# Performance work log

Measured on AMD Instinct MI355X. Metric: run time of the kernel, lower is better.

The kernel has to match this reference:

```python
import jax, jax.numpy as jnp
import numpy as np

B, T, C = 4, 4096, 1024
NEG_INF = -1e38


def setup_inputs() -> dict:
    key = jax.random.key(0)
    ks = jax.random.split(key, 5)
    scale = 0.02  # realistic init scale for CxC projections
    x = jax.random.normal(ks[0], (B, T, C), dtype=jnp.float32)
    key_w = jax.random.normal(ks[1], (C, C), dtype=jnp.float32) * scale
    value_w = jax.random.normal(ks[2], (C, C), dtype=jnp.float32) * scale
    receptance_w = jax.random.normal(ks[3], (C, C), dtype=jnp.float32) * scale
    output_w = jax.random.normal(ks[4], (C, C), dtype=jnp.float32) * scale
    # deterministic param init matching the module's __init__
    time_decay = -5.0 + 8.0 * (jnp.arange(C, dtype=jnp.float32) / (C - 1)) ** 0.7
    time_first = jnp.full((C,), -3.0, dtype=jnp.float32)
    # initial WKV state as in forward() when state is None
    aa0 = jnp.zeros((B, C), dtype=jnp.float32)
    bb0 = jnp.zeros((B, C), dtype=jnp.float32)
    pp0 = jnp.full((B, C), NEG_INF, dtype=jnp.float32)
    return dict(x=x, key_w=key_w, value_w=value_w, receptance_w=receptance_w,
                output_w=output_w, time_decay=time_decay, time_first=time_first,
                aa0=aa0, bb0=bb0, pp0=pp0)


def reference(x, key_w, value_w, receptance_w, output_w,
              time_decay, time_first, aa0, bb0, pp0):
    # projections (torch Linear: y = x @ W.T)
    k = jnp.einsum('btc,dc->btd', x, key_w)        # [B,T,C]
    v = jnp.einsum('btc,dc->btd', x, value_w)      # [B,T,C]
    r = jax.nn.sigmoid(jnp.einsum('btc,dc->btd', x, receptance_w))
    w = jnp.exp(time_decay)  # [C]
    u = time_first           # [C]

    def step(carry, kv):
        aa, bb, pp = carry           # each [B,C]
        kt, vt = kv                  # each [B,C]
        # output at this step (numerically stabilized exp weighting)
        ww = u + kt
        p = jnp.maximum(pp, ww)
        e1 = jnp.exp(pp - p)
        e2 = jnp.exp(ww - p)
        wkv = (e1 * aa + e2 * vt) / (e1 * bb + e2)
        # state update
        ww2 = pp - w
        p2 = jnp.maximum(ww2, kt)
        e1b = jnp.exp(ww2 - p2)
        e2b = jnp.exp(kt - p2)
        return (e1b * aa + e2b * vt, e1b * bb + e2b, p2), wkv

    k_t = jnp.swapaxes(k, 0, 1)  # [T,B,C]
    v_t = jnp.swapaxes(v, 0, 1)
    (aa, bb, pp), wkv = jax.lax.scan(step, (aa0, bb0, pp0), (k_t, v_t))
    wkv = jnp.swapaxes(wkv, 0, 1)  # [B,T,C]

    out = jnp.einsum('btc,dc->btd', r * wkv, output_w)
    return out, aa, bb, pp
```

## Files before the change

kernel.cpp:

```cpp
#include <hip/hip_runtime.h>
#include <stdint.h>

#define BDIM 4
#define TDIM 4096
#define CDIM 1024
#define MDIM (BDIM * TDIM)
#define SSEG 64
#define LSEG 64
#define NCH  (BDIM * CDIM)

#define GK   1024
#define GK2  2048
#define NTK  16
#define NT4  64

typedef __attribute__((ext_vector_type(8))) short bf16x8;
typedef __attribute__((ext_vector_type(4))) float f32x4;

__device__ __forceinline__ unsigned short f2bf(float f) {
    unsigned u = __builtin_bit_cast(unsigned, f);
    u = u + 0x7fffu + ((u >> 16) & 1u);
    return (unsigned short)(u >> 16);
}
__device__ __forceinline__ float bf2f(unsigned short h) {
    unsigned u = ((unsigned)h) << 16;
    return __builtin_bit_cast(float, u);
}

typedef __attribute__((address_space(1))) const unsigned int g_u32;
typedef __attribute__((address_space(3))) unsigned int l_u32;
__device__ __forceinline__ void gload_lds16(const void* g, void* l) {
    __builtin_amdgcn_global_load_lds((g_u32*)g, (l_u32*)l, 16, 0, 0);
}

__global__ void castk(const float* __restrict__ src, unsigned short* __restrict__ dst, int n4) {
    int i = blockIdx.x * blockDim.x + threadIdx.x;
    int stride = gridDim.x * blockDim.x;
    for (int j = i; j < n4; j += stride) {
        float4 f = ((const float4*)src)[j];
        ushort4 o;
        o.x = f2bf(f.x); o.y = f2bf(f.y); o.z = f2bf(f.z); o.w = f2bf(f.w);
        ((ushort4*)dst)[j] = o;
    }
}

template <int MODE>
__global__ __launch_bounds__(512, 2) void gemm256(
    const unsigned short* __restrict__ A,
    const unsigned short* __restrict__ Bw,
    unsigned short* __restrict__ oK, unsigned short* __restrict__ oV,
    unsigned short* __restrict__ oR, float* __restrict__ oF)
{
    extern __shared__ char sh[];
    char* shA = sh;
    char* shB = sh + 65536;

    const int tid  = threadIdx.x;
    const int wave = tid >> 6;
    const int lane = tid & 63;
    const int wm   = wave >> 2;
    const int wn   = wave & 3;
    const int lrow = lane & 15;
    const int koct = lane >> 4;

    const int nwg = gridDim.x;
    const int cpx = nwg >> 3;
    const int bid = blockIdx.x;
    const int wg  = (bid & 7) * cpx + (bid >> 3);
    const int mt  = wg & 63;
    const int nt  = wg >> 6;
    const size_t row0 = (size_t)mt * 256;
    const size_t col0 = (size_t)nt * 256;

    const char* gA = (const char*)A  + row0 * GK2;
    const char* gB = (const char*)Bw + col0 * GK2;

    auto stage_half = [&](int h) {
        if (h >= NT4) return;
        int t = h >> 2, part = h & 3, slot = t & 1;
        int isA = part >> 1, half = part & 1;
        const char* gbase = isA ? gA : gB;
        char* lbase = (isA ? shA : shB) + (slot * 2 + half) * 16384;
#pragma unroll
        for (int j = 0; j < 2; ++j) {
            int d = (j * 512 + tid) * 16;
            int r = d >> 7;
            int cb = (d & 127) ^ ((r & 7) << 4);
            gload_lds16(gbase + (size_t)(half * 128 + r) * GK2 + t * 128 + cb, lbase + d);
        }
    };

#pragma unroll
    for (int h = 0; h < 7; ++h) stage_half(h);
    asm volatile("s_waitcnt vmcnt(6)" ::: "memory");
    asm volatile("s_barrier" ::: "memory");

    f32x4 acc[8][4] = {};
    bf16x8 afr[8][2], bfr[4][2];

    for (int t = 0; t < NTK; ++t) {
        const int slot = t & 1;
        const int aoff = (slot * 2 + wm) * 16384;
        const int boff = (slot * 2 + (wn >> 1)) * 16384;
        const int brb  = (wn & 1) * 64;

#pragma unroll
        for (int mi = 0; mi < 4; ++mi) {
            int r = mi * 16 + lrow, sw = (r & 7) << 4;
#pragma unroll
            for (int ks = 0; ks < 2; ++ks)
                afr[mi][ks] = *(const bf16x8*)(shA + aoff + r * 128 + ((ks * 64 + koct * 16) ^ sw));
        }
#pragma unroll
        for (int ni = 0; ni < 4; ++ni) {
            int r = brb + ni * 16 + lrow, sw = (r & 7) << 4;
#pragma unroll
            for (int ks = 0; ks < 2; ++ks)
                bfr[ni][ks] = *(const bf16x8*)(shB + boff + r * 128 + ((ks * 64 + koct * 16) ^ sw));
        }
        stage_half(4 * t + 7);
        asm volatile("s_barrier" ::: "memory");
        __builtin_amdgcn_s_setprio(1);
#pragma unroll
        for (int a = 0; a < 4; ++a)
#pragma unroll
            for (int b = 0; b < 2; ++b)
#pragma unroll
                for (int ks = 0; ks < 2; ++ks)
                    acc[a][b] = __builtin_amdgcn_mfma_f32_16x16x32_bf16(afr[a][ks], bfr[b][ks], acc[a][b], 0, 0, 0);
        __builtin_amdgcn_s_setprio(0);
        asm volatile("s_barrier" ::: "memory");

#pragma unroll
        for (int mi = 4; mi < 8; ++mi) {
            int r = mi * 16 + lrow, sw = (r & 7) << 4;
#pragma unroll
            for (int ks = 0; ks < 2; ++ks)
                afr[mi][ks] = *(const bf16x8*)(shA + aoff + r * 128 + ((ks * 64 + koct * 16) ^ sw));
        }
        stage_half(4 * t + 8);
        asm volatile("s_barrier" ::: "memory");
        __builtin_amdgcn_s_setprio(1);
#pragma unroll
        for (int a = 0; a < 4; ++a)
#pragma unroll
            for (int b = 0; b < 2; ++b)
#pragma unroll
                for (int ks = 0; ks < 2; ++ks)
                    acc[a][2 + b] = __builtin_amdgcn_mfma_f32_16x16x32_bf16(afr[a][ks], bfr[2 + b][ks], acc[a][2 + b], 0, 0, 0);
        __builtin_amdgcn_s_setprio(0);
        asm volatile("s_barrier" ::: "memory");

        stage_half(4 * t + 9);
        asm volatile("s_barrier" ::: "memory");
        __builtin_amdgcn_s_setprio(1);
#pragma unroll
        for (int a = 0; a < 4; ++a)
#pragma unroll
            for (int b = 0; b < 2; ++b)
#pragma unroll
                for (int ks = 0; ks < 2; ++ks)
                    acc[4 + a][b] = __builtin_amdgcn_mfma_f32_16x16x32_bf16(afr[4 + a][ks], bfr[b][ks], acc[4 + a][b], 0, 0, 0);
        __builtin_amdgcn_s_setprio(0);
        asm volatile("s_barrier" ::: "memory");

        stage_half(4 * t + 10);
        asm volatile("s_barrier" ::: "memory");
        __builtin_amdgcn_s_setprio(1);
#pragma unroll
        for (int a = 0; a < 4; ++a)
#pragma unroll
            for (int b = 0; b < 2; ++b)
#pragma unroll
                for (int ks = 0; ks < 2; ++ks)
                    acc[4 + a][2 + b] = __builtin_amdgcn_mfma_f32_16x16x32_bf16(afr[4 + a][ks], bfr[2 + b][ks], acc[4 + a][2 + b], 0, 0, 0);
        __builtin_amdgcn_s_setprio(0);
        if (t < NTK - 2)       asm volatile("s_waitcnt vmcnt(6)" ::: "memory");
        else if (t == NTK - 2) asm volatile("s_waitcnt vmcnt(0)" ::: "memory");
        asm volatile("s_barrier" ::: "memory");
    }

    const int crow = (lane >> 4) * 4;
    const int ccol = lane & 15;
    if (MODE == 1) {
#pragma unroll
        for (int mi = 0; mi < 8; ++mi)
#pragma unroll
            for (int ni = 0; ni < 4; ++ni) {
                size_t gr = row0 + wm * 128 + mi * 16 + crow;
                size_t gc = col0 + wn * 64 + ni * 16 + ccol;
#pragma unroll
                for (int j = 0; j < 4; ++j)
                    oF[(gr + j) * 1024 + gc] = acc[mi][ni][j];
            }
    } else {
        const int region = nt >> 2;
        unsigned short* dst = (region == 0) ? oK : ((region == 1) ? oV : oR);
        const size_t cb0 = (size_t)(nt & 3) * 256;
#pragma unroll
        for (int mi = 0; mi < 8; ++mi)
#pragma unroll
            for (int ni = 0; ni < 4; ++ni) {
                size_t gr = row0 + wm * 128 + mi * 16 + crow;
                size_t gc = cb0 + wn * 64 + ni * 16 + ccol;
#pragma unroll
                for (int j = 0; j < 4; ++j) {
                    float val = acc[mi][ni][j];
                    if (region == 2) val = 1.0f / (1.0f + __expf(-val));
                    dst[(gr + j) * 1024 + gc] = f2bf(val);
                }
            }
    }
}

__global__ __launch_bounds__(256) void wkv_phase1(
    const unsigned short* __restrict__ kf, const unsigned short* __restrict__ vf,
    const float* __restrict__ td,
    float* __restrict__ segA, float* __restrict__ segB, float* __restrict__ segP)
{
    const int tid  = blockIdx.x * 256 + threadIdx.x;
    const int lane = tid & 63;
    const int wg   = tid >> 6;
    const int cg   = wg & 63;
    const int s    = wg >> 6;
    const int q    = cg * 64 + lane;
    const int b    = q >> 10;
    const int c    = q & (CDIM - 1);

    const float w = __expf(td[c]);

    float aa = 0.0f, bb = 0.0f, pp = -1e38f;
    size_t idx = (size_t)b * TDIM * CDIM + (size_t)(s * LSEG) * CDIM + c;
#pragma unroll 4
    for (int i = 0; i < LSEG; ++i, idx += CDIM) {
        float kt = bf2f(kf[idx]);
        float vt = bf2f(vf[idx]);
        float ww2 = pp - w;
        float p2  = fmaxf(ww2, kt);
        float e1  = __expf(ww2 - p2);
        float e2  = __expf(kt - p2);
        aa = e1 * aa + e2 * vt;
        bb = e1 * bb + e2;
        pp = p2;
    }
    segA[s * NCH + q] = aa;
    segB[s * NCH + q] = bb;
    segP[s * NCH + q] = pp;
}

__global__ __launch_bounds__(256) void wkv_phase2(
    const float* __restrict__ segA, const float* __restrict__ segB, const float* __restrict__ segP,
    const float* __restrict__ td,
    const float* __restrict__ aa0, const float* __restrict__ bb0, const float* __restrict__ pp0,
    float* __restrict__ preA, float* __restrict__ preB, float* __restrict__ preP,
    float* __restrict__ stout)
{
    const int tid = blockIdx.x * 256 + threadIdx.x;
    const int c = tid & (CDIM - 1);
    const float w  = __expf(td[c]);
    const float Lw = (float)LSEG * w;

    float aa = aa0[tid], bb = bb0[tid], pp = pp0[tid];
    for (int s = 0; s < SSEG; ++s) {
        preA[s * NCH + tid] = aa;
        preB[s * NCH + tid] = bb;
        preP[s * NCH + tid] = pp;
        float al = segA[s * NCH + tid];
        float bl = segB[s * NCH + tid];
        float pl = segP[s * NCH + tid];
        float ppd = pp - Lw;
        float p  = fmaxf(ppd, pl);
        float e1 = __expf(ppd - p);
        float e2 = __expf(pl - p);
        aa = e1 * aa + e2 * al;
        bb = e1 * bb + e2 * bl;
        pp = p;
    }
    stout[tid]           = aa;
    stout[NCH + tid]     = bb;
    stout[2 * NCH + tid] = pp;
}

__global__ __launch_bounds__(256) void wkv_phase3(
    const unsigned short* __restrict__ kf, const unsigned short* __restrict__ vf,
    const unsigned short* __restrict__ rb,
    const float* __restrict__ td, const float* __restrict__ tf,
    const float* __restrict__ preA, const float* __restrict__ preB, const float* __restrict__ preP,
    unsigned short* __restrict__ rwkvb)
{
    const int tid  = blockIdx.x * 256 + threadIdx.x;
    const int lane = tid & 63;
    const int wg   = tid >> 6;
    const int cg   = wg & 63;
    const int s    = wg >> 6;
    const int q    = cg * 64 + lane;
    const int b    = q >> 10;
    const int c    = q & (CDIM - 1);

    const float w = __expf(td[c]);
    const float u = tf[c];

    float aa = preA[s * NCH + q];
    float bb = preB[s * NCH + q];
    float pp = preP[s * NCH + q];

    size_t idx = (size_t)b * TDIM * CDIM + (size_t)(s * LSEG) * CDIM + c;
#pragma unroll 4
    for (int i = 0; i < LSEG; ++i, idx += CDIM) {
        float kt = bf2f(kf[idx]);
        float vt = bf2f(vf[idx]);
        float rt = bf2f(rb[idx]);
        float ww = u + kt;
        float p  = fmaxf(pp, ww);
        float e1 = __expf(pp - p);
        float e2 = __expf(ww - p);
        float wkv = (e1 * aa + e2 * vt) / (e1 * bb + e2);
        rwkvb[idx] = f2bf(rt * wkv);
        float ww2 = pp - w;
        float p2  = fmaxf(ww2, kt);
        float e1b = __expf(ww2 - p2);
        float e2b = __expf(kt - p2);
        aa = e1b * aa + e2b * vt;
        bb = e1b * bb + e2b;
        pp = p2;
    }
}

extern "C" void kernel_launch(void* const* d_in, const int* in_sizes, int n_in,
                              void* d_out, int out_size, void* d_ws, size_t ws_size,
                              hipStream_t stream) {
    const float* x   = (const float*)d_in[0];
    const float* kw  = (const float*)d_in[1];
    const float* vw  = (const float*)d_in[2];
    const float* rw  = (const float*)d_in[3];
    const float* ow  = (const float*)d_in[4];
    const float* td  = (const float*)d_in[5];
    const float* tf  = (const float*)d_in[6];
    const float* aa0 = (const float*)d_in[7];
    const float* bb0 = (const float*)d_in[8];
    const float* pp0 = (const float*)d_in[9];
    float* out = (float*)d_out;

    char* ws = (char*)d_ws;
    unsigned short* wf    = (unsigned short*)(ws);
    unsigned short* owb   = (unsigned short*)(ws + 6291456);
    unsigned short* xb    = (unsigned short*)(ws + 8388608);
    unsigned short* kfb   = (unsigned short*)(ws + 41943040);
    unsigned short* vfb   = (unsigned short*)(ws + 75497472);
    unsigned short* rbb   = (unsigned short*)(ws + 109051904);
    unsigned short* rwkvb = (unsigned short*)(ws + 142606336);
    float* segA = (float*)(ws + 176160768);
    float* segB = (float*)(ws + 177209344);
    float* segP = (float*)(ws + 178257920);
    float* preA = (float*)(ws + 179306496);
    float* preB = (float*)(ws + 180355072);
    float* preP = (float*)(ws + 181403648);

    hipFuncSetAttribute((const void*)gemm256<0>, hipFuncAttributeMaxDynamicSharedMemorySize, 131072);
    hipFuncSetAttribute((const void*)gemm256<1>, hipFuncAttributeMaxDynamicSharedMemorySize, 131072);

    castk<<<2048, 256, 0, stream>>>(x,  xb, MDIM * CDIM / 4);
    castk<<<512,  256, 0, stream>>>(kw, wf,            CDIM * CDIM / 4);
    castk<<<512,  256, 0, stream>>>(vw, wf + 1048576,  CDIM * CDIM / 4);
    castk<<<512,  256, 0, stream>>>(rw, wf + 2097152,  CDIM * CDIM / 4);
    castk<<<512,  256, 0, stream>>>(ow, owb,           CDIM * CDIM / 4);

    gemm256<0><<<768, 512, 131072, stream>>>(xb, wf, kfb, vfb, rbb, nullptr);

    wkv_phase1<<<NCH * SSEG / 256, 256, 0, stream>>>(kfb, vfb, td, segA, segB, segP);
    wkv_phase2<<<NCH / 256, 256, 0, stream>>>(segA, segB, segP, td, aa0, bb0, pp0,
                                              preA, preB, preP, out + (size_t)MDIM * CDIM);
    wkv_phase3<<<NCH * SSEG / 256, 256, 0, stream>>>(kfb, vfb, rbb, td, tf,
                                                     preA, preB, preP, rwkvb);

    gemm256<1><<<256, 512, 131072, stream>>>(rwkvb, owb, nullptr, nullptr, nullptr, out);
}
```

Measured before the change: 245.8 us.

## Restructure GEMM prefetch schedule and merge weight cast kernels

The GEMM main loop's global-to-LDS staging order is reworked. Next-tile B halves and the tile-after-next A halves are issued at different phases, and the first A fragments for the next k-step are loaded from LDS during the last MFMA phase of the current step, to hide LDS latency. The vmcnt waits are retuned to match. Separately, the four weight cast launches are merged into one castw kernel to cut launch overhead. The new staging distances could race or add register pressure if the wait counts are off.

New measurement: 241.3 us. Within noise of the previous version (-1.8%).

```diff
diff --git a/kernel.cpp b/kernel.cpp
--- a/kernel.cpp
+++ b/kernel.cpp
@@ -12,7 +12,6 @@
 #define GK   1024
 #define GK2  2048
 #define NTK  16
-#define NT4  64
 
 typedef __attribute__((ext_vector_type(8))) short bf16x8;
 typedef __attribute__((ext_vector_type(4))) float f32x4;
@@ -42,6 +41,19 @@
         o.x = f2bf(f.x); o.y = f2bf(f.y); o.z = f2bf(f.z); o.w = f2bf(f.w);
         ((ushort4*)dst)[j] = o;
     }
+}
+
+__global__ void castw(const float* __restrict__ kw, const float* __restrict__ vw,
+                      const float* __restrict__ rw, const float* __restrict__ ow,
+                      unsigned short* __restrict__ wf, unsigned short* __restrict__ owb) {
+    int i = blockIdx.x * 256 + threadIdx.x;
+    int m = i >> 18, j = i & 262143;
+    const float* s = (m == 0) ? kw : (m == 1) ? vw : (m == 2) ? rw : ow;
+    unsigned short* d = (m < 3) ? (wf + (size_t)m * 1048576) : owb;
+    float4 f = ((const float4*)s)[j];
+    ushort4 o;
+    o.x = f2bf(f.x); o.y = f2bf(f.y); o.z = f2bf(f.z); o.w = f2bf(f.w);
+    ((ushort4*)d)[j] = o;
 }
 
 template <int MODE>
@@ -75,10 +87,11 @@
     const char* gA = (const char*)A  + row0 * GK2;
     const char* gB = (const char*)Bw + col0 * GK2;
 
-    auto stage_half = [&](int h) {
-        if (h >= NT4) return;
-        int t = h >> 2, part = h & 3, slot = t & 1;
-        int isA = part >> 1, half = part & 1;
+    auto stage = [&](int tt, int part) {
+        if (tt >= NTK) return;
+        int slot = tt & 1;
+        int isA  = (part < 2) ? 1 : 0;
+        int half = part & 1;
         const char* gbase = isA ? gA : gB;
         char* lbase = (isA ? shA : shB) + (slot * 2 + half) * 16384;
 #pragma unroll
@@ -86,39 +99,48 @@
             int d = (j * 512 + tid) * 16;
             int r = d >> 7;
             int cb = (d & 127) ^ ((r & 7) << 4);
-            gload_lds16(gbase + (size_t)(half * 128 + r) * GK2 + t * 128 + cb, lbase + d);
+            gload_lds16(gbase + (size_t)(half * 128 + r) * GK2 + tt * 128 + cb, lbase + d);
         }
     };
 
-#pragma unroll
-    for (int h = 0; h < 7; ++h) stage_half(h);
-    asm volatile("s_waitcnt vmcnt(6)" ::: "memory");
+    stage(0, 0); stage(0, 1); stage(0, 2); stage(0, 3);
+    stage(1, 0); stage(1, 1);
+    asm volatile("s_waitcnt vmcnt(4)" ::: "memory");
     asm volatile("s_barrier" ::: "memory");
 
     f32x4 acc[8][4] = {};
-    bf16x8 afr[8][2], bfr[4][2];
-
-    for (int t = 0; t < NTK; ++t) {
-        const int slot = t & 1;
-        const int aoff = (slot * 2 + wm) * 16384;
-        const int boff = (slot * 2 + (wn >> 1)) * 16384;
-        const int brb  = (wn & 1) * 64;
-
+    bf16x8 afr[8], bfr[4];
+    bf16x8 afr2[8][1];
+    (void)afr2;
+    bf16x8 af[8][2], bf_[4][2];
+
+    {
+        const int aoff = (0 * 2 + wm) * 16384;
 #pragma unroll
         for (int mi = 0; mi < 4; ++mi) {
             int r = mi * 16 + lrow, sw = (r & 7) << 4;
 #pragma unroll
             for (int ks = 0; ks < 2; ++ks)
-                afr[mi][ks] = *(const bf16x8*)(shA + aoff + r * 128 + ((ks * 64 + koct * 16) ^ sw));
+                af[mi][ks] = *(const bf16x8*)(shA + aoff + r * 128 + ((ks * 64 + koct * 16) ^ sw));
         }
+    }
+
+    for (int t = 0; t < NTK; ++t) {
+        const int slot  = t & 1;
+        const int aoff  = (slot * 2 + wm) * 16384;
+        const int boff  = (slot * 2 + (wn >> 1)) * 16384;
+        const int brb   = (wn & 1) * 64;
+        const int slotN = (t + 1) & 1;
+        const int aoffN = (slotN * 2 + wm) * 16384;
+
+        stage(t + 1, 2);
 #pragma unroll
         for (int ni = 0; ni < 4; ++ni) {
             int r = brb + ni * 16 + lrow, sw = (r & 7) << 4;
 #pragma unroll
             for (int ks = 0; ks < 2; ++ks)
-                bfr[ni][ks] = *(const bf16x8*)(shB + boff + r * 128 + ((ks * 64 + koct * 16) ^ sw));
+                bf_[ni][ks] = *(const bf16x8*)(shB + boff + r * 128 + ((ks * 64 + koct * 16) ^ sw));
         }
-        stage_half(4 * t + 7);
         asm volatile("s_barrier" ::: "memory");
         __builtin_amdgcn_s_setprio(1);
 #pragma unroll
@@ -127,18 +149,18 @@
             for (int b = 0; b < 2; ++b)
 #pragma unroll
                 for (int ks = 0; ks < 2; ++ks)
-                    acc[a][b] = __builtin_amdgcn_mfma_f32_16x16x32_bf16(afr[a][ks], bfr[b][ks], acc[a][b], 0, 0, 0);
+                    acc[a][b] = __builtin_amdgcn_mfma_f32_16x16x32_bf16(af[a][ks], bf_[b][ks], acc[a][b], 0, 0, 0);
         __builtin_amdgcn_s_setprio(0);
         asm volatile("s_barrier" ::: "memory");
 
+        stage(t + 1, 3);
 #pragma unroll
         for (int mi = 4; mi < 8; ++mi) {
             int r = mi * 16 + lrow, sw = (r & 7) << 4;
 #pragma unroll
             for (int ks = 0; ks < 2; ++ks)
-                afr[mi][ks] = *(const bf16x8*)(shA + aoff + r * 128 + ((ks * 64 + koct * 16) ^ sw));
+                af[mi][ks] = *(const bf16x8*)(shA + aoff + r * 128 + ((ks * 64 + koct * 16) ^ sw));
         }
-        stage_half(4 * t + 8);
         asm volatile("s_barrier" ::: "memory");
         __builtin_amdgcn_s_setprio(1);
 #pragma unroll
@@ -147,11 +169,11 @@
             for (int b = 0; b < 2; ++b)
 #pragma unroll
                 for (int ks = 0; ks < 2; ++ks)
-                    acc[a][2 + b] = __builtin_amdgcn_mfma_f32_16x16x32_bf16(afr[a][ks], bfr[2 + b][ks], acc[a][2 + b], 0, 0, 0);
+                    acc[a][2 + b] = __builtin_amdgcn_mfma_f32_16x16x32_bf16(af[a][ks], bf_[2 + b][ks], acc[a][2 + b], 0, 0, 0);
         __builtin_amdgcn_s_setprio(0);
         asm volatile("s_barrier" ::: "memory");
 
-        stage_half(4 * t + 9);
+        stage(t + 2, 0);
         asm volatile("s_barrier" ::: "memory");
         __builtin_amdgcn_s_setprio(1);
 #pragma unroll
@@ -160,11 +182,22 @@
             for (int b = 0; b < 2; ++b)
 #pragma unroll
                 for (int ks = 0; ks < 2; ++ks)
-                    acc[4 + a][b] = __builtin_amdgcn_mfma_f32_16x16x32_bf16(afr[4 + a][ks], bfr[b][ks], acc[4 + a][b], 0, 0, 0);
+                    acc[4 + a][b] = __builtin_amdgcn_mfma_f32_16x16x32_bf16(af[4 + a][ks], bf_[b][ks], acc[4 + a][b], 0, 0, 0);
         __builtin_amdgcn_s_setprio(0);
-        asm volatile("s_barrier" ::: "memory");
-
-        stage_half(4 * t + 10);
+        if (t <= 13)      asm volatile("s_waitcnt vmcnt(6)" ::: "memory");
+        else if (t == 14) asm volatile("s_waitcnt vmcnt(4)" ::: "memory");
+        asm volatile("s_barrier" ::: "memory");
+
+        stage(t + 2, 1);
+        if (t + 1 < NTK) {
+#pragma unroll
+            for (int mi = 0; mi < 4; ++mi) {
+                int r = mi * 16 + lrow, sw = (r & 7) << 4;
+#pragma unroll
+                for (int ks = 0; ks < 2; ++ks)
+                    af[mi][ks] = *(const bf16x8*)(shA + aoffN + r * 128 + ((ks * 64 + koct * 16) ^ sw));
+            }
+        }
         asm volatile("s_barrier" ::: "memory");
         __builtin_amdgcn_s_setprio(1);
 #pragma unroll
@@ -173,10 +206,10 @@
             for (int b = 0; b < 2; ++b)
 #pragma unroll
                 for (int ks = 0; ks < 2; ++ks)
-                    acc[4 + a][2 + b] = __builtin_amdgcn_mfma_f32_16x16x32_bf16(afr[4 + a][ks], bfr[2 + b][ks], acc[4 + a][2 + b], 0, 0, 0);
+                    acc[4 + a][2 + b] = __builtin_amdgcn_mfma_f32_16x16x32_bf16(af[4 + a][ks], bf_[2 + b][ks], acc[4 + a][2 + b], 0, 0, 0);
         __builtin_amdgcn_s_setprio(0);
-        if (t < NTK - 2)       asm volatile("s_waitcnt vmcnt(6)" ::: "memory");
-        else if (t == NTK - 2) asm volatile("s_waitcnt vmcnt(0)" ::: "memory");
+        if (t <= 13)      asm volatile("s_waitcnt vmcnt(4)" ::: "memory");
+        else if (t == 14) asm volatile("s_waitcnt vmcnt(0)" ::: "memory");
         asm volatile("s_barrier" ::: "memory");
     }
 
@@ -359,11 +392,8 @@
     hipFuncSetAttribute((const void*)gemm256<0>, hipFuncAttributeMaxDynamicSharedMemorySize, 131072);
     hipFuncSetAttribute((const void*)gemm256<1>, hipFuncAttributeMaxDynamicSharedMemorySize, 131072);
 
-    castk<<<2048, 256, 0, stream>>>(x,  xb, MDIM * CDIM / 4);
-    castk<<<512,  256, 0, stream>>>(kw, wf,            CDIM * CDIM / 4);
-    castk<<<512,  256, 0, stream>>>(vw, wf + 1048576,  CDIM * CDIM / 4);
-    castk<<<512,  256, 0, stream>>>(rw, wf + 2097152,  CDIM * CDIM / 4);
-    castk<<<512,  256, 0, stream>>>(ow, owb,           CDIM * CDIM / 4);
+    castk<<<2048, 256, 0, stream>>>(x, xb, MDIM * CDIM / 4);
+    castw<<<4096, 256, 0, stream>>>(kw, vw, rw, ow, wf, owb);
 
     gemm256<0><<<768, 512, 131072, stream>>>(xb, wf, kfb, vfb, rbb, nullptr);
 
```
